# Optimization experiments

Hardware: AMD Instinct MI355X
Metric: run time of the kernel (lower is better)

## Reference

```python
import jax, jax.numpy as jnp
from jax import lax
import numpy as np

# ITA requantization params (from init_kwargs)
MQ, SQ = 16384, 8
MK, SK = 16384, 8
MV, SV = 16384, 8
MA, SA = 5, 12
MAV, SAV = 1, 8
MO, SO = 256, 7
NUM_HEADS = 6


def requantize(x, mult, shift, add=0):
    # x * mult, floor-div by 2**shift, add, clamp to int8 range (values kept in float32)
    return jnp.clip(jnp.floor(x * mult / (2.0 ** shift)) + add, -128.0, 127.0)


def ita_softmax(x):
    # x: [B, h, S, Skv] float32 with integer values in [-128, 127]
    B, h, S, Skv = x.shape
    width, bits = 16, 8
    eps_max = 32.0 * bits / (2 ** bits)  # range_scale * bits / 2**bits = 1.0
    groups = Skv // width
    x3 = x.reshape(B * h, S, Skv).astype(jnp.int32)
    # [groups, BH, S, width] for streaming scan over key chunks
    chunks = x3.reshape(B * h, S, groups, width).transpose(2, 0, 1, 3)

    def step(carry, chunk):
        exp_partial_sum, global_max = carry
        current_max = chunk.max(axis=-1)
        update = current_max > global_max
        max_shift = jnp.floor((current_max - global_max).astype(jnp.float32) * eps_max + 0.5).astype(jnp.int32)
        shift_sum = jnp.where(update, max_shift, 0)
        global_max = jnp.where(update, current_max, global_max)
        diff = global_max[..., None] - chunk  # >= 0
        shift = jnp.floor(diff.astype(jnp.float32) * eps_max + 0.5).astype(jnp.int32)
        # 2**bits >> shift  (256 >> shift; any shift >= 9 yields 0, clamp to keep shift defined)
        exp_sum = jnp.sum(jnp.right_shift(jnp.int32(256), jnp.minimum(shift, 31)), axis=-1).astype(jnp.int32)
        exp_partial_sum = jnp.right_shift(exp_partial_sum, jnp.minimum(shift_sum, 31)) + exp_sum
        return (exp_partial_sum, global_max), None

    init = (jnp.zeros((B * h, S), jnp.int32), jnp.full((B * h, S), -128, jnp.int32))
    (exp_partial_sum, global_max), _ = lax.scan(step, init, chunks)

    # (2**bits - 1) * 2**bits = 65280
    inv = jnp.floor(65280.0 / exp_partial_sum.astype(jnp.float32)).astype(jnp.int32)
    diff = global_max[..., None] - x3  # >= 0
    shift = jnp.floor(diff.astype(jnp.float32) * eps_max + 0.5).astype(jnp.int32)
    res = jnp.right_shift(inv[..., None], jnp.minimum(shift, 31)).astype(jnp.uint8)
    return res.reshape(B, h, S, Skv)


def setup_inputs() -> dict:
    key = jax.random.key(0)
    ks = jax.random.split(key, 9)
    B, N, D = 4, 2048, 384
    scale = 1.0 / np.sqrt(D)
    return {
        "x": jax.random.normal(ks[0], (B, N, D), jnp.float32),
        "wq": jax.random.normal(ks[1], (D, D), jnp.float32) * scale,
        "bq": jnp.zeros((D,), jnp.float32),
        "wk": jax.random.normal(ks[2], (D, D), jnp.float32) * scale,
        "bk": jnp.zeros((D,), jnp.float32),
        "wv": jax.random.normal(ks[3], (D, D), jnp.float32) * scale,
        "bv": jnp.zeros((D,), jnp.float32),
        "wo": jax.random.normal(ks[4], (D, D), jnp.float32) * scale,
        "bo": jnp.zeros((D,), jnp.float32),
        "H": 64,
        "W": 32,
    }


def reference(x, wq, bq, wk, bk, wv, bv, wo, bo, H, W):
    B, N, _ = x.shape
    h = NUM_HEADS
    hd = wq.shape[0] // h

    Q = requantize(x @ wq.T + bq, MQ, SQ)
    K = requantize(x @ wk.T + bk, MK, SK)
    V = requantize(x @ wv.T + bv, MV, SV)

    Qr = Q.reshape(B, N, h, hd).transpose(0, 2, 1, 3)  # [B,h,N,hd]
    Kr = K.reshape(B, N, h, hd).transpose(0, 2, 1, 3)
    Vr = V.reshape(B, N, h, hd).transpose(0, 2, 1, 3)

    logits = requantize(jnp.einsum('bhqd,bhkd->bhqk', Qr, Kr), MA, SA)
    attn = ita_softmax(logits)  # uint8 [B,h,N,N]
    ctx = requantize(jnp.einsum('bhqk,bhkd->bhqd', attn.astype(jnp.float32), Vr), MAV, SAV)
    ctx = ctx.transpose(0, 2, 1, 3).reshape(B, N, h * hd)
    out = requantize(ctx @ wo.T + bo, MO, SO)
    return out
```

## Files before the change

kernel.cpp:

```cpp
#include <hip/hip_runtime.h>
#include <stdint.h>

#define NB 4
#define NN 2048
#define ND 384
#define NH 6
#define HD 64
#define ROWS (NB * NN)

typedef int v4i __attribute__((ext_vector_type(4)));

__global__ __launch_bounds__(256) void qkv_gemm_kernel(
    const float* __restrict__ X,
    const float* __restrict__ Wq, const float* __restrict__ Wk, const float* __restrict__ Wv,
    const float* __restrict__ Bq, const float* __restrict__ Bk, const float* __restrict__ Bv,
    int8_t* __restrict__ Q8, int8_t* __restrict__ K8, int8_t* __restrict__ V8T,
    int* __restrict__ CS)
{
    __shared__ float As[16][132];
    __shared__ float Bs[16][76];
    __shared__ int lcol[64];

    const int t = threadIdx.x;
    const int row0 = blockIdx.x * 128;
    const int c0g = blockIdx.y * 64;
    const int m = c0g / ND;
    const int cl0 = c0g - m * ND;
    const float* W = (m == 0) ? Wq : (m == 1) ? Wk : Wv;
    const float* Bi = (m == 0) ? Bq : (m == 1) ? Bk : Bv;

    const int tx = t & 15;
    const int ty = t >> 4;
    const int lr = t >> 1;
    const int kh = (t & 1) * 8;
    const int rb = t >> 2;
    const int kb = (t & 3) * 4;

    float acc[8][4];
#pragma unroll
    for (int i = 0; i < 8; i++)
#pragma unroll
        for (int j = 0; j < 4; j++) acc[i][j] = 0.f;

    const float* xrow = X + (size_t)(row0 + lr) * ND + kh;
    const float* wrow = W + (size_t)(cl0 + rb) * ND + kb;

    for (int k0 = 0; k0 < ND; k0 += 16) {
        float4 a0 = *(const float4*)(xrow + k0);
        float4 a1 = *(const float4*)(xrow + k0 + 4);
        float4 b0 = *(const float4*)(wrow + k0);
        As[kh + 0][lr] = a0.x; As[kh + 1][lr] = a0.y; As[kh + 2][lr] = a0.z; As[kh + 3][lr] = a0.w;
        As[kh + 4][lr] = a1.x; As[kh + 5][lr] = a1.y; As[kh + 6][lr] = a1.z; As[kh + 7][lr] = a1.w;
        Bs[kb + 0][rb] = b0.x; Bs[kb + 1][rb] = b0.y; Bs[kb + 2][rb] = b0.z; Bs[kb + 3][rb] = b0.w;
        __syncthreads();
#pragma unroll
        for (int kk = 0; kk < 16; kk++) {
            float4 av0 = *(const float4*)&As[kk][ty * 8];
            float4 av1 = *(const float4*)&As[kk][ty * 8 + 4];
            float4 bv  = *(const float4*)&Bs[kk][tx * 4];
            float a[8] = {av0.x, av0.y, av0.z, av0.w, av1.x, av1.y, av1.z, av1.w};
            float b[4] = {bv.x, bv.y, bv.z, bv.w};
#pragma unroll
            for (int i = 0; i < 8; i++)
#pragma unroll
                for (int j = 0; j < 4; j++)
                    acc[i][j] += a[i] * b[j];
        }
        __syncthreads();
    }

    const int bidx = row0 >> 11;
    const int n0 = row0 & 2047;
    const int head = cl0 >> 6;
    if (m == 2) {
        if (t < 64) lcol[t] = 0;
        __syncthreads();
#pragma unroll
        for (int j = 0; j < 4; j++) {
            const int dim = tx * 4 + j;
            const float bias = Bi[cl0 + dim];
            int s = 0;
            uint32_t w[2] = {0u, 0u};
#pragma unroll
            for (int i = 0; i < 8; i++) {
                float v = acc[i][j] + bias;
                int qv = (int)floorf(v * 64.0f);
                qv = max(-128, min(127, qv));
                s += qv;
                w[i >> 2] |= (uint32_t)(qv & 255) << (8 * (i & 3));
            }
            uint32_t* dst = (uint32_t*)(V8T + (((size_t)(bidx * NH + head) * HD + dim) * NN
                                              + n0 + ty * 8));
            dst[0] = w[0];
            dst[1] = w[1];
            atomicAdd(&lcol[dim], s);
        }
        __syncthreads();
        if (t < 64)
            atomicAdd(&CS[(bidx * NH + head) * 64 + t], lcol[t]);
    } else {
        int8_t* Out = (m == 0) ? Q8 : K8;
#pragma unroll
        for (int i = 0; i < 8; i++) {
            const int n = n0 + ty * 8 + i;
            uint32_t w = 0;
#pragma unroll
            for (int j = 0; j < 4; j++) {
                float v = acc[i][j] + Bi[cl0 + tx * 4 + j];
                int qv = (int)floorf(v * 64.0f);
                qv = max(-128, min(127, qv));
                w |= (uint32_t)(qv & 255) << (8 * j);
            }
            *(uint32_t*)(Out + (((size_t)(bidx * NH + head) * NN) + n) * HD + tx * 4) = w;
        }
    }
}

__global__ __launch_bounds__(256, 3) void attn_kernel(
    const int8_t* __restrict__ Q8, const int8_t* __restrict__ K8,
    const int8_t* __restrict__ V8T, const int* __restrict__ colsum,
    int8_t* __restrict__ CTX8)
{
    __shared__ int Lp[128 * 68];
    __shared__ int stats[2 * 16 * 132];
    __shared__ int invq[16];
    __shared__ int gmq[16];

    int* gmax = stats;
    int* esum = stats + 16 * 132;

    const int t = threadIdx.x;
    const int wid = t >> 6;
    const int lane = t & 63;
    const int quad = lane >> 4;
    const int l15 = lane & 15;
    const int bh = blockIdx.y;
    const int q0 = blockIdx.x * 16;
    const size_t base = (size_t)bh * NN * HD;
    const v4i zero = {0, 0, 0, 0};

    v4i afrag = *(const v4i*)(Q8 + base + (size_t)(q0 + l15) * HD + quad * 16);
    for (int kt = wid * 32; kt < wid * 32 + 32; ++kt) {
        v4i bfrag = *(const v4i*)(K8 + base + (size_t)(kt * 16 + l15) * HD + quad * 16);
        v4i d = __builtin_amdgcn_mfma_i32_16x16x64_i8(afrag, bfrag, zero, 0, 0, 0);
        int w = 0;
#pragma unroll
        for (int r = 0; r < 4; ++r) {
            int lg = (d[r] * 5) >> 12;
            lg = min(127, max(-128, lg));
            w |= (lg & 255) << (8 * r);
        }
        Lp[kt * 68 + quad * 16 + l15] = w;
    }
    __syncthreads();

#pragma unroll
    for (int it = 0; it < 2; ++it) {
        const int task = t + it * 256;
        const int g = task & 127, qq = task >> 7;
        const int* p = &Lp[g * 68 + qq * 16];
        int wb[16];
#pragma unroll
        for (int a = 0; a < 4; ++a) {
            v4i v = *(const v4i*)&p[a * 4];
            wb[a * 4 + 0] = v.x; wb[a * 4 + 1] = v.y; wb[a * 4 + 2] = v.z; wb[a * 4 + 3] = v.w;
        }
#pragma unroll
        for (int b = 0; b < 4; ++b) {
            int mx = INT_MIN;
#pragma unroll
            for (int j = 0; j < 16; ++j)
                mx = max(mx, (int)((unsigned)wb[j] << (8 * (3 - b))));
            gmax[(qq * 4 + b) * 132 + g] = (mx >> 24);
        }
    }
    __syncthreads();

    if (t < 16) {
        int m = -128;
        for (int g4 = 0; g4 < 128; g4 += 4) {
            v4i v = *(v4i*)&gmax[t * 132 + g4];
            m = max(m, v.x); v.x = m;
            m = max(m, v.y); v.y = m;
            m = max(m, v.z); v.z = m;
            m = max(m, v.w); v.w = m;
            *(v4i*)&gmax[t * 132 + g4] = v;
        }
    }
    __syncthreads();

#pragma unroll
    for (int it = 0; it < 2; ++it) {
        const int task = t + it * 256;
        const int g = task & 127, qq = task >> 7;
        const int* p = &Lp[g * 68 + qq * 16];
        int wb[16];
#pragma unroll
        for (int a = 0; a < 4; ++a) {
            v4i v = *(const v4i*)&p[a * 4];
            wb[a * 4 + 0] = v.x; wb[a * 4 + 1] = v.y; wb[a * 4 + 2] = v.z; wb[a * 4 + 3] = v.w;
        }
#pragma unroll
        for (int b = 0; b < 4; ++b) {
            const int M = gmax[(qq * 4 + b) * 132 + g];
            const int cb = 8 - M;
            int s = 0;
#pragma unroll
            for (int j = 0; j < 16; ++j) {
                int x = (int)(int8_t)(wb[j] >> (8 * b));
                int tt = x + cb;
                s += (tt >= 0) ? (1 << tt) : 0;
            }
            esum[(qq * 4 + b) * 132 + g] = s;
        }
    }
    __syncthreads();

    if (t < 16) {
        int E = 0, Mp = -128;
        for (int g = 0; g < 128; ++g) {
            int m = gmax[t * 132 + g];
            int d = m - Mp; if (d > 31) d = 31;
            E = (E >> d) + esum[t * 132 + g];
            Mp = m;
        }
        invq[t] = 65280 / E;
        gmq[t] = Mp;
    }
    __syncthreads();

    {
        const int qw = t & 3;
        const int k15 = (t >> 2) & 15;
        const int band = t >> 6;
        int c24[4]; unsigned invv[4];
#pragma unroll
        for (int b = 0; b < 4; ++b) {
            c24[b] = 24 - gmq[qw * 4 + b];
            invv[b] = (unsigned)invq[qw * 4 + b];
        }
        for (int j = 0; j < 32; ++j) {
            const int kt = band * 32 + j;
            const int idx = kt * 68 + qw * 16 + k15;
            const int w = Lp[idx];
            unsigned outw = 0;
#pragma unroll
            for (int b = 0; b < 4; ++b) {
                int x = (int)(int8_t)(w >> (8 * b));
                int t1 = x + c24[b];
                t1 = (t1 < 0) ? 0 : t1;
                unsigned a = (invv[b] << t1) >> 24;
                outw |= ((a - 128u) & 255u) << (8 * b);
            }
            Lp[idx] = (int)outw;
        }
    }
    __syncthreads();

    const int sh8 = 8 * (l15 & 3);
    v4i accs[4] = {zero, zero, zero, zero};
    const int8_t* vtb = V8T + base;

    for (int kc = wid * 8; kc < wid * 8 + 8; ++kc) {
        const int* lp = &Lp[(kc * 4 + quad) * 68 + (l15 >> 2) * 16];
        v4i a;
#pragma unroll
        for (int r = 0; r < 4; ++r) {
            const int w0 = lp[4 * r + 0], w1 = lp[4 * r + 1];
            const int w2 = lp[4 * r + 2], w3 = lp[4 * r + 3];
            a[r] = (int)((((unsigned)w0 >> sh8) & 255u) |
                         ((((unsigned)w1 >> sh8) & 255u) << 8) |
                         ((((unsigned)w2 >> sh8) & 255u) << 16) |
                         ((((unsigned)w3 >> sh8) & 255u) << 24));
        }
        const int koff = kc * 64 + quad * 16;
        v4i b0 = *(const v4i*)(vtb + (size_t)(0 * 16 + l15) * NN + koff);
        v4i b1 = *(const v4i*)(vtb + (size_t)(1 * 16 + l15) * NN + koff);
        v4i b2 = *(const v4i*)(vtb + (size_t)(2 * 16 + l15) * NN + koff);
        v4i b3 = *(const v4i*)(vtb + (size_t)(3 * 16 + l15) * NN + koff);
        accs[0] = __builtin_amdgcn_mfma_i32_16x16x64_i8(a, b0, accs[0], 0, 0, 0);
        accs[1] = __builtin_amdgcn_mfma_i32_16x16x64_i8(a, b1, accs[1], 0, 0, 0);
        accs[2] = __builtin_amdgcn_mfma_i32_16x16x64_i8(a, b2, accs[2], 0, 0, 0);
        accs[3] = __builtin_amdgcn_mfma_i32_16x16x64_i8(a, b3, accs[3], 0, 0, 0);
    }
    __syncthreads();

    if (wid > 0) {
#pragma unroll
        for (int dt = 0; dt < 4; ++dt)
#pragma unroll
            for (int r = 0; r < 4; ++r)
                stats[(dt * 4 + r) * 192 + (wid - 1) * 64 + lane] = accs[dt][r];
    }
    __syncthreads();
    if (wid == 0) {
        const int bb = bh / NH, hh = bh % NH;
        const int* cs = &colsum[bh * 64];
#pragma unroll
        for (int dt = 0; dt < 4; ++dt) {
            const int dcol = dt * 16 + l15;
            const int corr = cs[dcol] << 7;
#pragma unroll
            for (int r = 0; r < 4; ++r) {
                const int i = dt * 4 + r;
                int val = accs[dt][r]
                        + stats[i * 192 + 0 * 64 + lane]
                        + stats[i * 192 + 1 * 64 + lane]
                        + stats[i * 192 + 2 * 64 + lane];
                const int q = q0 + quad * 4 + r;
                val = (val + corr) >> 8;
                val = min(127, max(-128, val));
                CTX8[((size_t)(bb * NN + q)) * ND + hh * HD + dcol] = (int8_t)val;
            }
        }
    }
}

__global__ __launch_bounds__(256) void out_gemm_kernel(
    const int8_t* __restrict__ CTX8, const float* __restrict__ Wo,
    const float* __restrict__ Bo, float* __restrict__ out)
{
    __shared__ float As[16][68];
    __shared__ float Bs[16][68];

    const int t = threadIdx.x;
    const int row0 = blockIdx.x * 64;
    const int c0 = blockIdx.y * 64;
    const int li = t >> 2;
    const int lk = (t & 3) << 2;
    const int tx = t & 15, ty = t >> 4;

    float acc[4][4] = {{0.f}};

    for (int k0 = 0; k0 < ND; k0 += 16) {
        const int av = *(const int*)&CTX8[(size_t)(row0 + li) * ND + k0 + lk];
        float4 b = *(const float4*)&Wo[(size_t)(c0 + li) * ND + k0 + lk];
        As[lk + 0][li] = (float)(int)(int8_t)(av & 0xFF);
        As[lk + 1][li] = (float)(int)(int8_t)((av >> 8) & 0xFF);
        As[lk + 2][li] = (float)(int)(int8_t)((av >> 16) & 0xFF);
        As[lk + 3][li] = (float)(int)(int8_t)((av >> 24) & 0xFF);
        Bs[lk + 0][li] = b.x; Bs[lk + 1][li] = b.y; Bs[lk + 2][li] = b.z; Bs[lk + 3][li] = b.w;
        __syncthreads();
#pragma unroll
        for (int kk = 0; kk < 16; kk++) {
            float4 avv = *(const float4*)&As[kk][ty * 4];
            float4 bvv = *(const float4*)&Bs[kk][tx * 4];
            float aa[4] = {avv.x, avv.y, avv.z, avv.w};
            float bb[4] = {bvv.x, bvv.y, bvv.z, bvv.w};
#pragma unroll
            for (int i = 0; i < 4; i++)
#pragma unroll
                for (int j = 0; j < 4; j++)
                    acc[i][j] += aa[i] * bb[j];
        }
        __syncthreads();
    }

#pragma unroll
    for (int i = 0; i < 4; i++) {
        const int r = row0 + ty * 4 + i;
#pragma unroll
        for (int j = 0; j < 4; j++) {
            const int c = c0 + tx * 4 + j;
            float v = acc[i][j] + Bo[c];
            float rq = floorf(v * 2.0f);
            rq = fminf(fmaxf(rq, -128.0f), 127.0f);
            out[(size_t)r * ND + c] = rq;
        }
    }
}

extern "C" void kernel_launch(void* const* d_in, const int* in_sizes, int n_in,
                              void* d_out, int out_size, void* d_ws, size_t ws_size,
                              hipStream_t stream)
{
    const float* x  = (const float*)d_in[0];
    const float* wq = (const float*)d_in[1];
    const float* bq = (const float*)d_in[2];
    const float* wk = (const float*)d_in[3];
    const float* bk = (const float*)d_in[4];
    const float* wv = (const float*)d_in[5];
    const float* bv = (const float*)d_in[6];
    const float* wo = (const float*)d_in[7];
    const float* bo = (const float*)d_in[8];
    float* out = (float*)d_out;

    const size_t MAT = (size_t)ROWS * ND;
    int8_t* Q8  = (int8_t*)d_ws;
    int8_t* K8  = Q8 + MAT;
    int8_t* V8T = K8 + MAT;
    int8_t* C8  = V8T + MAT;
    int*    CS  = (int*)(C8 + MAT);

    hipMemsetAsync(CS, 0, (size_t)NB * NH * 64 * sizeof(int), stream);
    qkv_gemm_kernel<<<dim3(ROWS / 128, 1152 / 64), 256, 0, stream>>>(
        x, wq, wk, wv, bq, bk, bv, Q8, K8, V8T, CS);
    attn_kernel<<<dim3(NN / 16, NB * NH), 256, 0, stream>>>(Q8, K8, V8T, CS, C8);
    out_gemm_kernel<<<dim3(ROWS / 64, ND / 64), 256, 0, stream>>>(C8, wo, bo, out);
}
```

Baseline: 311.2 us.

## Fuse softmax normalization into PV operand build and shrink attention LDS footprint

Per-chunk max and exp-sum statistics are now packed as bytes and 16-bit halves instead of full ints, and the final reduction scratch reuses the logits buffer. This cuts LDS per block enough to raise launch bounds from 3 to 4 blocks per SIMD. The separate normalization pass over the logits tile, with its extra barrier, is removed. Instead each lane computes the shifted probabilities while assembling MFMA A-operands, using byte-permute instructions. The cost is that the shift work is now repeated inside the PV loop, and the 16-bit exp-sum packing relies on each chunk sum staying below 65536.

```diff
diff --git a/kernel.cpp b/kernel.cpp
--- a/kernel.cpp
+++ b/kernel.cpp
@@ -116,18 +116,14 @@
     }
 }
 
-__global__ __launch_bounds__(256, 3) void attn_kernel(
+__global__ __launch_bounds__(256, 4) void attn_kernel(
     const int8_t* __restrict__ Q8, const int8_t* __restrict__ K8,
     const int8_t* __restrict__ V8T, const int* __restrict__ colsum,
     int8_t* __restrict__ CTX8)
 {
     __shared__ int Lp[128 * 68];
-    __shared__ int stats[2 * 16 * 132];
-    __shared__ int invq[16];
-    __shared__ int gmq[16];
-
-    int* gmax = stats;
-    int* esum = stats + 16 * 132;
+    __shared__ int gmaxw[128 * 4];
+    __shared__ int esumw[128 * 8];
 
     const int t = threadIdx.x;
     const int wid = t >> 6;
@@ -143,14 +139,15 @@
     for (int kt = wid * 32; kt < wid * 32 + 32; ++kt) {
         v4i bfrag = *(const v4i*)(K8 + base + (size_t)(kt * 16 + l15) * HD + quad * 16);
         v4i d = __builtin_amdgcn_mfma_i32_16x16x64_i8(afrag, bfrag, zero, 0, 0, 0);
-        int w = 0;
+        int e[4];
 #pragma unroll
         for (int r = 0; r < 4; ++r) {
             int lg = (d[r] * 5) >> 12;
-            lg = min(127, max(-128, lg));
-            w |= (lg & 255) << (8 * r);
-        }
-        Lp[kt * 68 + quad * 16 + l15] = w;
+            e[r] = min(127, max(-128, lg));
+        }
+        int p01 = __builtin_amdgcn_perm(e[1], e[0], 0x00000400);
+        int p23 = __builtin_amdgcn_perm(e[3], e[2], 0x00000400);
+        Lp[kt * 68 + quad * 16 + l15] = __builtin_amdgcn_perm(p23, p01, 0x05040100);
     }
     __syncthreads();
 
@@ -165,26 +162,29 @@
             v4i v = *(const v4i*)&p[a * 4];
             wb[a * 4 + 0] = v.x; wb[a * 4 + 1] = v.y; wb[a * 4 + 2] = v.z; wb[a * 4 + 3] = v.w;
         }
+        int mx[4];
 #pragma unroll
         for (int b = 0; b < 4; ++b) {
-            int mx = INT_MIN;
+            int m = INT_MIN;
 #pragma unroll
             for (int j = 0; j < 16; ++j)
-                mx = max(mx, (int)((unsigned)wb[j] << (8 * (3 - b))));
-            gmax[(qq * 4 + b) * 132 + g] = (mx >> 24);
-        }
+                m = max(m, (int)((unsigned)wb[j] << (8 * (3 - b))));
+            mx[b] = m;
+        }
+        int p01 = __builtin_amdgcn_perm(mx[1], mx[0], 0x00000703);
+        int p23 = __builtin_amdgcn_perm(mx[3], mx[2], 0x00000703);
+        gmaxw[g * 4 + qq] = __builtin_amdgcn_perm(p23, p01, 0x05040100);
     }
     __syncthreads();
 
     if (t < 16) {
+        const int wq = t >> 2, bq = 8 * (t & 3);
+        int8_t* gb = (int8_t*)gmaxw;
         int m = -128;
-        for (int g4 = 0; g4 < 128; g4 += 4) {
-            v4i v = *(v4i*)&gmax[t * 132 + g4];
-            m = max(m, v.x); v.x = m;
-            m = max(m, v.y); v.y = m;
-            m = max(m, v.z); v.z = m;
-            m = max(m, v.w); v.w = m;
-            *(v4i*)&gmax[t * 132 + g4] = v;
+        for (int g = 0; g < 128; ++g) {
+            int x = (int)(int8_t)(gmaxw[g * 4 + wq] >> bq);
+            m = max(m, x);
+            gb[g * 16 + t] = (int8_t)m;
         }
     }
     __syncthreads();
@@ -200,9 +200,11 @@
             v4i v = *(const v4i*)&p[a * 4];
             wb[a * 4 + 0] = v.x; wb[a * 4 + 1] = v.y; wb[a * 4 + 2] = v.z; wb[a * 4 + 3] = v.w;
         }
+        const int pw = gmaxw[g * 4 + qq];
+        uint32_t sp[2] = {0u, 0u};
 #pragma unroll
         for (int b = 0; b < 4; ++b) {
-            const int M = gmax[(qq * 4 + b) * 132 + g];
+            const int M = (int)(int8_t)(pw >> (8 * b));
             const int cb = 8 - M;
             int s = 0;
 #pragma unroll
@@ -211,52 +213,29 @@
                 int tt = x + cb;
                 s += (tt >= 0) ? (1 << tt) : 0;
             }
-            esum[(qq * 4 + b) * 132 + g] = s;
-        }
+            sp[b >> 1] |= (uint32_t)s << (16 * (b & 1));
+        }
+        *(int2*)&esumw[g * 8 + qq * 2] = make_int2((int)sp[0], (int)sp[1]);
     }
     __syncthreads();
 
     if (t < 16) {
+        const int8_t* gb = (const int8_t*)gmaxw;
+        const uint16_t* eb = (const uint16_t*)esumw;
         int E = 0, Mp = -128;
         for (int g = 0; g < 128; ++g) {
-            int m = gmax[t * 132 + g];
+            int m = (int)gb[g * 16 + t];
             int d = m - Mp; if (d > 31) d = 31;
-            E = (E >> d) + esum[t * 132 + g];
+            E = (E >> d) + (int)eb[g * 16 + t];
             Mp = m;
         }
-        invq[t] = 65280 / E;
-        gmq[t] = Mp;
-    }
-    __syncthreads();
-
-    {
-        const int qw = t & 3;
-        const int k15 = (t >> 2) & 15;
-        const int band = t >> 6;
-        int c24[4]; unsigned invv[4];
-#pragma unroll
-        for (int b = 0; b < 4; ++b) {
-            c24[b] = 24 - gmq[qw * 4 + b];
-            invv[b] = (unsigned)invq[qw * 4 + b];
-        }
-        for (int j = 0; j < 32; ++j) {
-            const int kt = band * 32 + j;
-            const int idx = kt * 68 + qw * 16 + k15;
-            const int w = Lp[idx];
-            unsigned outw = 0;
-#pragma unroll
-            for (int b = 0; b < 4; ++b) {
-                int x = (int)(int8_t)(w >> (8 * b));
-                int t1 = x + c24[b];
-                t1 = (t1 < 0) ? 0 : t1;
-                unsigned a = (invv[b] << t1) >> 24;
-                outw |= ((a - 128u) & 255u) << (8 * b);
-            }
-            Lp[idx] = (int)outw;
-        }
-    }
-    __syncthreads();
-
+        Lp[t * 68 + 64] = 65280 / E;
+        Lp[t * 68 + 65] = Mp;
+    }
+    __syncthreads();
+
+    const int inv_l = Lp[l15 * 68 + 64];
+    const int c24 = 24 - Lp[l15 * 68 + 65];
     const int sh8 = 8 * (l15 & 3);
     v4i accs[4] = {zero, zero, zero, zero};
     const int8_t* vtb = V8T + base;
@@ -266,12 +245,18 @@
         v4i a;
 #pragma unroll
         for (int r = 0; r < 4; ++r) {
-            const int w0 = lp[4 * r + 0], w1 = lp[4 * r + 1];
-            const int w2 = lp[4 * r + 2], w3 = lp[4 * r + 3];
-            a[r] = (int)((((unsigned)w0 >> sh8) & 255u) |
-                         ((((unsigned)w1 >> sh8) & 255u) << 8) |
-                         ((((unsigned)w2 >> sh8) & 255u) << 16) |
-                         ((((unsigned)w3 >> sh8) & 255u) << 24));
+            v4i w4 = *(const v4i*)&lp[4 * r];
+            int u[4];
+#pragma unroll
+            for (int c = 0; c < 4; ++c) {
+                int x = (int)(int8_t)(w4[c] >> sh8);
+                int t1 = x + c24;
+                t1 = (t1 < 0) ? 0 : t1;
+                u[c] = (int)((unsigned)inv_l << t1);
+            }
+            int p01 = __builtin_amdgcn_perm(u[1], u[0], 0x00000703);
+            int p23 = __builtin_amdgcn_perm(u[3], u[2], 0x00000703);
+            a[r] = __builtin_amdgcn_perm(p23, p01, 0x05040100) ^ (int)0x80808080u;
         }
         const int koff = kc * 64 + quad * 16;
         v4i b0 = *(const v4i*)(vtb + (size_t)(0 * 16 + l15) * NN + koff);
@@ -290,7 +275,7 @@
         for (int dt = 0; dt < 4; ++dt)
 #pragma unroll
             for (int r = 0; r < 4; ++r)
-                stats[(dt * 4 + r) * 192 + (wid - 1) * 64 + lane] = accs[dt][r];
+                Lp[(dt * 4 + r) * 192 + (wid - 1) * 64 + lane] = accs[dt][r];
     }
     __syncthreads();
     if (wid == 0) {
@@ -304,9 +289,9 @@
             for (int r = 0; r < 4; ++r) {
                 const int i = dt * 4 + r;
                 int val = accs[dt][r]
-                        + stats[i * 192 + 0 * 64 + lane]
-                        + stats[i * 192 + 1 * 64 + lane]
-                        + stats[i * 192 + 2 * 64 + lane];
+                        + Lp[i * 192 + 0 * 64 + lane]
+                        + Lp[i * 192 + 1 * 64 + lane]
+                        + Lp[i * 192 + 2 * 64 + lane];
                 const int q = q0 + quad * 4 + r;
                 val = (val + corr) >> 8;
                 val = min(127, max(-128, val));
```

Measured after the change: 304.0 us. 1.02x faster.
